# Kernel optimization log

Hardware: AMD Instinct MI355X
Metric: run time of the kernel (lower is better)

Reference implementation:

```python
import jax, jax.numpy as jnp
import numpy as np

B, S, D_MODEL, H = 4, 4096, 1024, 16
HD = D_MODEL // H  # head_dim = 64


def setup_inputs() -> dict:
    key = jax.random.key(0)
    kq, kk, kv, kw, kb = jax.random.split(key, 5)
    Q = jax.random.normal(kq, (B, S, D_MODEL), dtype=jnp.float32)
    K = jax.random.normal(kk, (B, S, D_MODEL), dtype=jnp.float32)
    V = jax.random.normal(kv, (B, S, D_MODEL), dtype=jnp.float32)
    # out_proj: nn.Linear(d_model, d_model)
    lim = 1.0 / np.sqrt(D_MODEL)
    W_out = jax.random.uniform(kw, (D_MODEL, D_MODEL), jnp.float32, -lim, lim)
    b_out = jax.random.uniform(kb, (D_MODEL,), jnp.float32, -lim, lim)
    return {"Q": Q, "K": K, "V": V, "W_out": W_out, "b_out": b_out}


def reference(Q, K, V, W_out, b_out):
    b, s, d = Q.shape
    # split heads: [B, H, S, HD]
    Qh = Q.reshape(b, s, H, HD).transpose(0, 2, 1, 3)
    Kh = K.reshape(b, s, H, HD).transpose(0, 2, 1, 3)
    Vh = V.reshape(b, s, H, HD).transpose(0, 2, 1, 3)
    # linear attention reorder: KV = K^T V -> [B, H, HD, HD]
    KV = jnp.einsum('bhsd,bhse->bhde', Kh, Vh)
    # z = Q @ KV -> [B, H, S, HD]
    z = jnp.einsum('bhsd,bhde->bhse', Qh, KV)
    # merge heads -> [B, S, D]
    z = z.transpose(0, 2, 1, 3).reshape(b, s, d)
    # out_proj (torch Linear: x @ W^T + b, here W_out stored [out,in])
    return z @ W_out.T + b_out
```

## Files before the change

### kernel.cpp

```cpp
#include <hip/hip_runtime.h>
#include <hip/hip_bf16.h>

#define B_ 4
#define S_ 4096
#define DM 1024
#define H_ 16
#define HD 64
#define BH (B_*H_)
#define SPLIT 8
#define CHUNK (S_/SPLIT)
#define SUB 64

typedef __attribute__((ext_vector_type(8))) __bf16 bf16x8;
typedef __attribute__((ext_vector_type(4))) __bf16 bf16x4;
typedef __attribute__((ext_vector_type(4))) float f32x4;

#define MFMA16(a,b,c) __builtin_amdgcn_mfma_f32_16x16x32_bf16((a),(b),(c),0,0,0)

__device__ __forceinline__ void gload_lds16(const void* g, void* l) {
  __builtin_amdgcn_global_load_lds(
      (const __attribute__((address_space(1))) void*)g,
      (__attribute__((address_space(3))) void*)l, 16, 0, 0);
}

__global__ __launch_bounds__(256)
void k0_convq(const float* __restrict__ Qg, __bf16* __restrict__ Qb) {
  const size_t t = (size_t)blockIdx.x * 256 + threadIdx.x;
#pragma unroll
  for (int it = 0; it < 4; ++it) {
    const size_t i = (size_t)it * 1048576 + t;
    f32x4 w = *reinterpret_cast<const f32x4*>(Qg + i * 4);
    bf16x4 o;
#pragma unroll
    for (int j = 0; j < 4; ++j) o[j] = (__bf16)w[j];
    *reinterpret_cast<bf16x4*>(Qb + i * 4) = o;
  }
}

__global__ __launch_bounds__(256)
void k1_kv(const float* __restrict__ Kg, const float* __restrict__ Vg,
           float* __restrict__ partial) {
  __shared__ __align__(16) float sh[16384];
  const int bid = blockIdx.x;
  const int split = bid >> 6, bh = bid & 63;
  const int b = bh >> 4, h = bh & 15;
  const int t = threadIdx.x, w = t >> 6, l = t & 63;
  const int s0 = split * CHUNK;
  const float* Ksrc = Kg + ((size_t)b * S_ + s0) * DM + h * HD;
  const float* Vsrc = Vg + ((size_t)b * S_ + s0) * DM + h * HD;
  const int td = (l >> 3) * 8, te = (l & 7) * 8;
  float acc[8][8] = {};

  auto stage = [&](int bi, int sc) {
    const char* Kp = (const char*)(Ksrc + (size_t)sc * SUB * DM);
    const char* Vp = (const char*)(Vsrc + (size_t)sc * SUB * DM);
    char* Kl = (char*)sh + bi * 16384;
    char* Vl = (char*)sh + 32768 + bi * 16384;
#pragma unroll
    for (int it = 0; it < 4; ++it) {
      const int idx = it * 256 + t;
      const int row = idx >> 4, ch = idx & 15;
      const int ldso = (it * 256 + w * 64) * 16;
      gload_lds16((const void*)(Kp + (size_t)row * 4096 + ch * 16), (void*)(Kl + ldso));
      gload_lds16((const void*)(Vp + (size_t)row * 4096 + ch * 16), (void*)(Vl + ldso));
    }
  };

  stage(0, 0);
  asm volatile("s_waitcnt vmcnt(0)" ::: "memory");
  __builtin_amdgcn_s_barrier();

  for (int hc = 0; hc < CHUNK / SUB; ++hc) {
    const int cur = hc & 1;
    if (hc + 1 < CHUNK / SUB) stage(cur ^ 1, hc + 1);
    const float* Ks = sh + cur * 4096;
    const float* Vs = sh + 8192 + cur * 4096;
#pragma unroll 4
    for (int si = 0; si < SUB / 4; ++si) {
      const int s = si * 4 + w;
      f32x4 ka = *reinterpret_cast<const f32x4*>(Ks + s * 64 + td);
      f32x4 kb = *reinterpret_cast<const f32x4*>(Ks + s * 64 + td + 4);
      f32x4 va = *reinterpret_cast<const f32x4*>(Vs + s * 64 + te);
      f32x4 vb = *reinterpret_cast<const f32x4*>(Vs + s * 64 + te + 4);
#pragma unroll
      for (int i = 0; i < 4; ++i)
#pragma unroll
        for (int j = 0; j < 4; ++j) {
          acc[i][j]         = fmaf(ka[i], va[j], acc[i][j]);
          acc[i][j + 4]     = fmaf(ka[i], vb[j], acc[i][j + 4]);
          acc[i + 4][j]     = fmaf(kb[i], va[j], acc[i + 4][j]);
          acc[i + 4][j + 4] = fmaf(kb[i], vb[j], acc[i + 4][j + 4]);
        }
    }
    asm volatile("s_waitcnt vmcnt(0)" ::: "memory");
    __builtin_amdgcn_s_barrier();
  }

  float* red = sh;
#pragma unroll
  for (int i = 0; i < 8; ++i)
#pragma unroll
    for (int jc = 0; jc < 2; ++jc) {
      f32x4 o;
#pragma unroll
      for (int j = 0; j < 4; ++j) o[j] = acc[i][jc * 4 + j];
      *reinterpret_cast<f32x4*>(red + w * 4096 + (td + i) * 64 + te + jc * 4) = o;
    }
  __builtin_amdgcn_s_barrier();
  float* dst = partial + ((size_t)(split * BH + bh) << 12);
#pragma unroll
  for (int c2 = 0; c2 < 4; ++c2) {
    const int base = (c2 * 256 + t) * 4;
    f32x4 a0 = *reinterpret_cast<const f32x4*>(red + base);
    f32x4 a1 = *reinterpret_cast<const f32x4*>(red + 4096 + base);
    f32x4 a2 = *reinterpret_cast<const f32x4*>(red + 8192 + base);
    f32x4 a3 = *reinterpret_cast<const f32x4*>(red + 12288 + base);
    f32x4 o;
#pragma unroll
    for (int j = 0; j < 4; ++j) o[j] = (a0[j] + a1[j]) + (a2[j] + a3[j]);
    *reinterpret_cast<f32x4*>(dst + base) = o;
  }
}

__global__ __launch_bounds__(256)
void k2_kv_reduce(const float* __restrict__ partial,
                  __bf16* __restrict__ kvt) {
  const int bid = blockIdx.x;
  const int bh = bid >> 2, q = bid & 3;
  const int t = threadIdx.x;
#pragma unroll
  for (int i = 0; i < 4; ++i) {
    const int idx = q * 1024 + i * 256 + t;
    float s = 0.f;
#pragma unroll
    for (int sp = 0; sp < SPLIT; ++sp)
      s += partial[((size_t)(sp * BH + bh) << 12) + idx];
    kvt[((size_t)bh << 12) + idx] = (__bf16)s;
  }
}

__global__ __launch_bounds__(256)
void k25_u(const float* __restrict__ Wg,
           const __bf16* __restrict__ kvt,
           __bf16* __restrict__ Ut) {
  const int bid = blockIdx.x;
  const int bh = bid >> 2, nblk = bid & 3;
  const int b = bh >> 4, h = bh & 15;
  const int t = threadIdx.x, w = t >> 6, l = t & 63, lr = l & 15, lg = l >> 4;
  const int n0w = nblk * 256 + w * 64;
  const __bf16* kvb = kvt + ((size_t)bh << 12);
  f32x4 acc[4][4] = {};
#pragma unroll
  for (int ks = 0; ks < 2; ++ks) {
    bf16x8 bfr[4];
#pragma unroll
    for (int nf = 0; nf < 4; ++nf)
      bfr[nf] = *reinterpret_cast<const bf16x8*>(kvb + (nf * 16 + lr) * 64 + ks * 32 + lg * 8);
#pragma unroll
    for (int mf = 0; mf < 4; ++mf) {
      const int n = n0w + mf * 16 + lr;
      const float* wp = Wg + (size_t)n * DM + h * 64 + ks * 32 + lg * 8;
      f32x4 w0 = *reinterpret_cast<const f32x4*>(wp);
      f32x4 w1 = *reinterpret_cast<const f32x4*>(wp + 4);
      bf16x8 af;
#pragma unroll
      for (int j = 0; j < 4; ++j) { af[j] = (__bf16)w0[j]; af[4 + j] = (__bf16)w1[j]; }
#pragma unroll
      for (int nf = 0; nf < 4; ++nf)
        acc[mf][nf] = MFMA16(af, bfr[nf], acc[mf][nf]);
    }
  }
  __bf16* ub = Ut + ((size_t)b << 20);
#pragma unroll
  for (int mf = 0; mf < 4; ++mf)
#pragma unroll
    for (int nf = 0; nf < 4; ++nf)
#pragma unroll
      for (int r = 0; r < 4; ++r) {
        const int n = n0w + mf * 16 + lg * 4 + r;
        ub[(size_t)n * DM + h * 64 + nf * 16 + lr] = (__bf16)acc[mf][nf][r];
      }
}

__global__ __launch_bounds__(256)
void k4_out_gemm(const __bf16* __restrict__ Qb,
                 const __bf16* __restrict__ Ut,
                 const float* __restrict__ biasg,
                 float* __restrict__ outg) {
  __shared__ __align__(16) __bf16 Alds[128 * 64];
  __shared__ __align__(16) __bf16 Blds[128 * 64];
  const int bid = blockIdx.x;
  const int b = bid >> 8, rem = bid & 255;
  const int nblk = rem >> 5, mblk = rem & 31;
  const int m0 = mblk * 128, n0 = nblk * 128;
  const int t = threadIdx.x, wid = t >> 6, l = t & 63, lr = l & 15, lg = l >> 4;
  const int wr = wid >> 1, wc = wid & 1;
  const __bf16* Ab = Qb + (size_t)b * S_ * DM;
  const __bf16* Bb = Ut + ((size_t)b << 20);
  f32x4 acc[4][4] = {};

  for (int kt = 0; kt < 16; ++kt) {
    const int k0 = kt * 64;
#pragma unroll
    for (int it = 0; it < 4; ++it) {
      const int idx = it * 256 + t;
      const int row = idx >> 3, c = idx & 7;
      const int gc = c ^ (row & 7);
      gload_lds16((const void*)(Ab + (size_t)(m0 + row) * DM + k0 + gc * 8),
                  (void*)((char*)Alds + (it * 256 + wid * 64) * 16));
      gload_lds16((const void*)(Bb + (size_t)(n0 + row) * DM + k0 + gc * 8),
                  (void*)((char*)Blds + (it * 256 + wid * 64) * 16));
    }
    __syncthreads();
#pragma unroll
    for (int ks = 0; ks < 2; ++ks) {
      bf16x8 af[4], bfr[4];
#pragma unroll
      for (int mt = 0; mt < 4; ++mt) {
        const int row = wr * 64 + mt * 16 + lr;
        const int ch = (ks * 4 + lg) ^ (row & 7);
        af[mt] = *reinterpret_cast<const bf16x8*>((const char*)Alds + row * 128 + ch * 16);
      }
#pragma unroll
      for (int nt = 0; nt < 4; ++nt) {
        const int row = wc * 64 + nt * 16 + lr;
        const int ch = (ks * 4 + lg) ^ (row & 7);
        bfr[nt] = *reinterpret_cast<const bf16x8*>((const char*)Blds + row * 128 + ch * 16);
      }
#pragma unroll
      for (int mt = 0; mt < 4; ++mt)
#pragma unroll
        for (int nt = 0; nt < 4; ++nt)
          acc[mt][nt] = MFMA16(af[mt], bfr[nt], acc[mt][nt]);
    }
    __syncthreads();
  }

#pragma unroll
  for (int nt = 0; nt < 4; ++nt) {
    const int colg = n0 + wc * 64 + nt * 16 + lr;
    const float bv = biasg[colg];
#pragma unroll
    for (int mt = 0; mt < 4; ++mt)
#pragma unroll
      for (int r = 0; r < 4; ++r) {
        const int rowg = m0 + wr * 64 + mt * 16 + lg * 4 + r;
        outg[((size_t)b * S_ + rowg) * DM + colg] = acc[mt][nt][r] + bv;
      }
  }
}

extern "C" void kernel_launch(void* const* d_in, const int* in_sizes, int n_in,
                              void* d_out, int out_size, void* d_ws, size_t ws_size,
                              hipStream_t stream) {
  const float* Q = (const float*)d_in[0];
  const float* K = (const float*)d_in[1];
  const float* V = (const float*)d_in[2];
  const float* W = (const float*)d_in[3];
  const float* bias = (const float*)d_in[4];
  float* out = (float*)d_out;

  char* ws = (char*)d_ws;
  float* partial = (float*)ws;
  __bf16* kvt = (__bf16*)(ws + (8u << 20));
  __bf16* Ut  = (__bf16*)(ws + (9u << 20));
  __bf16* Qb  = (__bf16*)(ws + (17u << 20));

  hipLaunchKernelGGL(k1_kv, dim3(SPLIT * BH), dim3(256), 0, stream, K, V, partial);
  hipLaunchKernelGGL(k0_convq, dim3(4096), dim3(256), 0, stream, Q, Qb);
  hipLaunchKernelGGL(k2_kv_reduce, dim3(BH * 4), dim3(256), 0, stream, partial, kvt);
  hipLaunchKernelGGL(k25_u, dim3(BH * 4), dim3(256), 0, stream, W, kvt, Ut);
  hipLaunchKernelGGL(k4_out_gemm, dim3(1024), dim3(256), 0, stream, Qb, Ut, bias, out);
}
```

Baseline: 128.1 us.

## Fuse Q bf16 conversion into output GEMM and shrink KV partial LDS

Removes the separate Q fp32-to-bf16 conversion kernel and instead loads fp32 Q tiles straight into LDS in the output GEMM, converting to bf16 at fragment-load time with an XOR swizzle. The KV partial kernel doubles SPLIT and halves SUB, which halves its LDS footprint and doubles the block count, and its final cross-wave reduction becomes a tree through a smaller LDS buffer. This drops a full write and re-read of bf16 Q, at the cost of twice the fp32 A bytes per GEMM tile, more LDS traffic, and twice as many partials to reduce.

```diff
diff --git a/kernel.cpp b/kernel.cpp
--- a/kernel.cpp
+++ b/kernel.cpp
@@ -7,9 +7,9 @@
 #define H_ 16
 #define HD 64
 #define BH (B_*H_)
-#define SPLIT 8
+#define SPLIT 16
 #define CHUNK (S_/SPLIT)
-#define SUB 64
+#define SUB 32
 
 typedef __attribute__((ext_vector_type(8))) __bf16 bf16x8;
 typedef __attribute__((ext_vector_type(4))) __bf16 bf16x4;
@@ -24,23 +24,9 @@
 }
 
 __global__ __launch_bounds__(256)
-void k0_convq(const float* __restrict__ Qg, __bf16* __restrict__ Qb) {
-  const size_t t = (size_t)blockIdx.x * 256 + threadIdx.x;
-#pragma unroll
-  for (int it = 0; it < 4; ++it) {
-    const size_t i = (size_t)it * 1048576 + t;
-    f32x4 w = *reinterpret_cast<const f32x4*>(Qg + i * 4);
-    bf16x4 o;
-#pragma unroll
-    for (int j = 0; j < 4; ++j) o[j] = (__bf16)w[j];
-    *reinterpret_cast<bf16x4*>(Qb + i * 4) = o;
-  }
-}
-
-__global__ __launch_bounds__(256)
 void k1_kv(const float* __restrict__ Kg, const float* __restrict__ Vg,
            float* __restrict__ partial) {
-  __shared__ __align__(16) float sh[16384];
+  __shared__ __align__(16) float sh[8192];
   const int bid = blockIdx.x;
   const int split = bid >> 6, bh = bid & 63;
   const int b = bh >> 4, h = bh & 15;
@@ -54,10 +40,10 @@
   auto stage = [&](int bi, int sc) {
     const char* Kp = (const char*)(Ksrc + (size_t)sc * SUB * DM);
     const char* Vp = (const char*)(Vsrc + (size_t)sc * SUB * DM);
-    char* Kl = (char*)sh + bi * 16384;
-    char* Vl = (char*)sh + 32768 + bi * 16384;
-#pragma unroll
-    for (int it = 0; it < 4; ++it) {
+    char* Kl = (char*)(sh + bi * 2048);
+    char* Vl = (char*)(sh + 4096 + bi * 2048);
+#pragma unroll
+    for (int it = 0; it < 2; ++it) {
       const int idx = it * 256 + t;
       const int row = idx >> 4, ch = idx & 15;
       const int ldso = (it * 256 + w * 64) * 16;
@@ -73,9 +59,9 @@
   for (int hc = 0; hc < CHUNK / SUB; ++hc) {
     const int cur = hc & 1;
     if (hc + 1 < CHUNK / SUB) stage(cur ^ 1, hc + 1);
-    const float* Ks = sh + cur * 4096;
-    const float* Vs = sh + 8192 + cur * 4096;
-#pragma unroll 4
+    const float* Ks = sh + cur * 2048;
+    const float* Vs = sh + 4096 + cur * 2048;
+#pragma unroll
     for (int si = 0; si < SUB / 4; ++si) {
       const int s = si * 4 + w;
       f32x4 ka = *reinterpret_cast<const f32x4*>(Ks + s * 64 + td);
@@ -97,28 +83,55 @@
   }
 
   float* red = sh;
-#pragma unroll
-  for (int i = 0; i < 8; ++i)
-#pragma unroll
-    for (int jc = 0; jc < 2; ++jc) {
-      f32x4 o;
-#pragma unroll
-      for (int j = 0; j < 4; ++j) o[j] = acc[i][jc * 4 + j];
-      *reinterpret_cast<f32x4*>(red + w * 4096 + (td + i) * 64 + te + jc * 4) = o;
-    }
-  __builtin_amdgcn_s_barrier();
-  float* dst = partial + ((size_t)(split * BH + bh) << 12);
-#pragma unroll
-  for (int c2 = 0; c2 < 4; ++c2) {
-    const int base = (c2 * 256 + t) * 4;
-    f32x4 a0 = *reinterpret_cast<const f32x4*>(red + base);
-    f32x4 a1 = *reinterpret_cast<const f32x4*>(red + 4096 + base);
-    f32x4 a2 = *reinterpret_cast<const f32x4*>(red + 8192 + base);
-    f32x4 a3 = *reinterpret_cast<const f32x4*>(red + 12288 + base);
-    f32x4 o;
-#pragma unroll
-    for (int j = 0; j < 4; ++j) o[j] = (a0[j] + a1[j]) + (a2[j] + a3[j]);
-    *reinterpret_cast<f32x4*>(dst + base) = o;
+  if (w >= 2) {
+    float* dl = red + (w - 2) * 4096;
+#pragma unroll
+    for (int i = 0; i < 8; ++i)
+#pragma unroll
+      for (int jc = 0; jc < 2; ++jc) {
+        f32x4 o;
+#pragma unroll
+        for (int j = 0; j < 4; ++j) o[j] = acc[i][jc * 4 + j];
+        *reinterpret_cast<f32x4*>(dl + (td + i) * 64 + te + jc * 4) = o;
+      }
+  }
+  __syncthreads();
+  if (w < 2) {
+    const float* sl = red + w * 4096;
+#pragma unroll
+    for (int i = 0; i < 8; ++i)
+#pragma unroll
+      for (int jc = 0; jc < 2; ++jc) {
+        f32x4 v = *reinterpret_cast<const f32x4*>(sl + (td + i) * 64 + te + jc * 4);
+#pragma unroll
+        for (int j = 0; j < 4; ++j) acc[i][jc * 4 + j] += v[j];
+      }
+  }
+  __syncthreads();
+  if (w == 1) {
+#pragma unroll
+    for (int i = 0; i < 8; ++i)
+#pragma unroll
+      for (int jc = 0; jc < 2; ++jc) {
+        f32x4 o;
+#pragma unroll
+        for (int j = 0; j < 4; ++j) o[j] = acc[i][jc * 4 + j];
+        *reinterpret_cast<f32x4*>(red + (td + i) * 64 + te + jc * 4) = o;
+      }
+  }
+  __syncthreads();
+  if (w == 0) {
+    float* dst = partial + ((size_t)(split * BH + bh) << 12);
+#pragma unroll
+    for (int i = 0; i < 8; ++i)
+#pragma unroll
+      for (int jc = 0; jc < 2; ++jc) {
+        f32x4 v = *reinterpret_cast<const f32x4*>(red + (td + i) * 64 + te + jc * 4);
+        f32x4 o;
+#pragma unroll
+        for (int j = 0; j < 4; ++j) o[j] = acc[i][jc * 4 + j] + v[j];
+        *reinterpret_cast<f32x4*>(dst + (td + i) * 64 + te + jc * 4) = o;
+      }
   }
 }
 
@@ -183,33 +196,39 @@
 }
 
 __global__ __launch_bounds__(256)
-void k4_out_gemm(const __bf16* __restrict__ Qb,
+void k4_out_gemm(const float* __restrict__ Qg,
                  const __bf16* __restrict__ Ut,
                  const float* __restrict__ biasg,
                  float* __restrict__ outg) {
-  __shared__ __align__(16) __bf16 Alds[128 * 64];
-  __shared__ __align__(16) __bf16 Blds[128 * 64];
+  __shared__ __align__(16) float Af[128 * 64];
+  __shared__ __align__(16) __bf16 Bl[128 * 64];
   const int bid = blockIdx.x;
   const int b = bid >> 8, rem = bid & 255;
   const int nblk = rem >> 5, mblk = rem & 31;
   const int m0 = mblk * 128, n0 = nblk * 128;
   const int t = threadIdx.x, wid = t >> 6, l = t & 63, lr = l & 15, lg = l >> 4;
   const int wr = wid >> 1, wc = wid & 1;
-  const __bf16* Ab = Qb + (size_t)b * S_ * DM;
+  const float* Ab = Qg + (size_t)b * S_ * DM;
   const __bf16* Bb = Ut + ((size_t)b << 20);
   f32x4 acc[4][4] = {};
 
   for (int kt = 0; kt < 16; ++kt) {
     const int k0 = kt * 64;
+#pragma unroll
+    for (int it = 0; it < 8; ++it) {
+      const int idx = it * 256 + t;
+      const int row = idx >> 4, g = idx & 15;
+      const int gc = g ^ ((row & 7) << 1);
+      gload_lds16((const void*)(Ab + (size_t)(m0 + row) * DM + k0 + gc * 4),
+                  (void*)((char*)Af + (it * 256 + wid * 64) * 16));
+    }
 #pragma unroll
     for (int it = 0; it < 4; ++it) {
       const int idx = it * 256 + t;
       const int row = idx >> 3, c = idx & 7;
       const int gc = c ^ (row & 7);
-      gload_lds16((const void*)(Ab + (size_t)(m0 + row) * DM + k0 + gc * 8),
-                  (void*)((char*)Alds + (it * 256 + wid * 64) * 16));
       gload_lds16((const void*)(Bb + (size_t)(n0 + row) * DM + k0 + gc * 8),
-                  (void*)((char*)Blds + (it * 256 + wid * 64) * 16));
+                  (void*)((char*)Bl + (it * 256 + wid * 64) * 16));
     }
     __syncthreads();
 #pragma unroll
@@ -218,14 +237,18 @@
 #pragma unroll
       for (int mt = 0; mt < 4; ++mt) {
         const int row = wr * 64 + mt * 16 + lr;
-        const int ch = (ks * 4 + lg) ^ (row & 7);
-        af[mt] = *reinterpret_cast<const bf16x8*>((const char*)Alds + row * 128 + ch * 16);
+        const int up = (ks * 4 + lg) ^ (row & 7);
+        const float* p = reinterpret_cast<const float*>((const char*)Af + row * 256 + up * 32);
+        f32x4 lo = *reinterpret_cast<const f32x4*>(p);
+        f32x4 hi = *reinterpret_cast<const f32x4*>(p + 4);
+#pragma unroll
+        for (int j = 0; j < 4; ++j) { af[mt][j] = (__bf16)lo[j]; af[mt][4 + j] = (__bf16)hi[j]; }
       }
 #pragma unroll
       for (int nt = 0; nt < 4; ++nt) {
         const int row = wc * 64 + nt * 16 + lr;
         const int ch = (ks * 4 + lg) ^ (row & 7);
-        bfr[nt] = *reinterpret_cast<const bf16x8*>((const char*)Blds + row * 128 + ch * 16);
+        bfr[nt] = *reinterpret_cast<const bf16x8*>((const char*)Bl + row * 128 + ch * 16);
       }
 #pragma unroll
       for (int mt = 0; mt < 4; ++mt)
@@ -262,13 +285,11 @@
 
   char* ws = (char*)d_ws;
   float* partial = (float*)ws;
-  __bf16* kvt = (__bf16*)(ws + (8u << 20));
-  __bf16* Ut  = (__bf16*)(ws + (9u << 20));
-  __bf16* Qb  = (__bf16*)(ws + (17u << 20));
+  __bf16* kvt = (__bf16*)(ws + (16u << 20));
+  __bf16* Ut  = (__bf16*)(ws + (17u << 20));
 
   hipLaunchKernelGGL(k1_kv, dim3(SPLIT * BH), dim3(256), 0, stream, K, V, partial);
-  hipLaunchKernelGGL(k0_convq, dim3(4096), dim3(256), 0, stream, Q, Qb);
   hipLaunchKernelGGL(k2_kv_reduce, dim3(BH * 4), dim3(256), 0, stream, partial, kvt);
   hipLaunchKernelGGL(k25_u, dim3(BH * 4), dim3(256), 0, stream, W, kvt, Ut);
-  hipLaunchKernelGGL(k4_out_gemm, dim3(1024), dim3(256), 0, stream, Qb, Ut, bias, out);
-}
+  hipLaunchKernelGGL(k4_out_gemm, dim3(1024), dim3(256), 0, stream, Q, Ut, bias, out);
+}
```

After: 141.7 us. 1.11x slower.
